# Performance work log

Measured on AMD Instinct MI355X. Metric: run time of the kernel, lower is better.

## Reference

```python
import jax, jax.numpy as jnp
import numpy as np

ATTR_W = 1.0   # attraction_weight
REP_W = 1.0    # repulsion_weight
K_INST = 64    # max number of slice (instance) ids per event


def setup_inputs() -> dict:
    key = jax.random.key(0)
    k1, k2, k3, k4 = jax.random.split(key, 4)
    B, N, D = 4, 4096, 8
    beta = jax.random.normal(k1, (B, N, 1), dtype=jnp.float32)
    embed = jax.random.normal(k2, (B, N, D), dtype=jnp.float32)
    slice_id = jax.random.randint(k3, (B, N), 0, K_INST)
    is_cp = jax.random.randint(k4, (B, N), 0, 2)
    return {"beta": beta, "embed": embed, "slice_id": slice_id, "is_cp": is_cp}


def _per_batch(beta_b, emb_b, sid, cp):
    # beta_b: [N], emb_b: [N, D], sid: [N] int, cp: [N] int
    N = beta_b.shape[0]
    cp_mask = cp == 1
    y = cp_mask.astype(beta_b.dtype)
    pos = jnp.sum(y)
    neg = N - pos
    valid = (pos >= 1) & (neg >= 1)
    # beta BCE-with-logits with detached pos_weight = neg/pos
    pos_weight = jax.lax.stop_gradient(neg / (pos + 1e-6))
    bce = jnp.mean(pos_weight * y * jax.nn.softplus(-beta_b)
                   + (1.0 - y) * jax.nn.softplus(beta_b))
    # attraction: per instance, mean squared distance to first CP hit of that instance
    idx = jnp.arange(N)
    first_cp = jax.ops.segment_min(jnp.where(cp_mask, idx, N), sid, num_segments=K_INST)
    has_cp = first_cp < N                                   # [K]
    cp_emb = emb_b[jnp.clip(first_cp, 0, N - 1)]            # [K, D]
    d2 = jnp.sum((emb_b - cp_emb[sid]) ** 2, axis=-1)       # [N]
    seg_sum = jax.ops.segment_sum(d2, sid, num_segments=K_INST)
    counts = jax.ops.segment_sum(jnp.ones((N,), beta_b.dtype), sid, num_segments=K_INST)
    inst_mean = jnp.where((counts > 0) & has_cp, seg_sum / jnp.maximum(counts, 1.0), 0.0)
    attr = jnp.sum(inst_mean) * ATTR_W
    # repulsion: mean of exp(-d2) over all CP x CP pairs (diagonal included)
    sq = jnp.sum(emb_b * emb_b, axis=-1)                    # [N]
    d2p = jnp.maximum(sq[:, None] + sq[None, :] - 2.0 * (emb_b @ emb_b.T), 0.0)  # [N, N]
    rep_sum = jnp.sum(jnp.exp(-d2p) * (y[:, None] * y[None, :]))
    rep = jnp.where(pos > 1, rep_sum / jnp.maximum(pos * pos, 1.0), 0.0) * REP_W
    total = bce + attr + rep
    return jnp.where(valid, total, 0.0), valid.astype(beta_b.dtype)


def reference(beta, embed, slice_id, is_cp):
    beta2 = beta.squeeze(-1)                                # [B, N]
    totals, valids = jax.vmap(_per_batch)(beta2, embed, slice_id, is_cp)
    count = jnp.sum(valids)
    return jnp.where(count > 0, jnp.sum(totals) / jnp.maximum(count, 1.0), 0.0)
```

## Files before the change

kernel.cpp:

```cpp
#include <hip/hip_runtime.h>
#include <math.h>

#define BB 4
#define NN 4096
#define KK 64
#define IT 1024
#define JT 32
#define K2_BLOCKS (BB * (NN/IT) * (NN/JT))

__global__ __launch_bounds__(1024) void k1(
    const float* __restrict__ beta, const float* __restrict__ embed,
    const int* __restrict__ sid_g, const int* __restrict__ cp_g,
    float* __restrict__ cpemb, float* __restrict__ cpsq,
    float* __restrict__ gbase, float* __restrict__ gpos,
    float* __restrict__ grep, int* __restrict__ gcpn)
{
    const int b    = blockIdx.x;
    const int t    = threadIdx.x;
    const int lane = t & 63;
    const int wid  = t >> 6;

    __shared__ int   s_first[KK];
    __shared__ int   s_counts[KK];
    __shared__ float s_seg[KK];
    __shared__ float s_fe[KK][8];
    __shared__ float r1[16], r2[16], r3[16];
    __shared__ int   s_cpn;

    if (t < KK) { s_first[t] = NN; s_counts[t] = 0; s_seg[t] = 0.f; }
    if (t == 0) s_cpn = 0;
    __syncthreads();

    const int4*   sid4 = (const int4*)(sid_g + (size_t)b * NN);
    const int4*   cp4  = (const int4*)(cp_g + (size_t)b * NN);
    const float4* bt4p = (const float4*)(beta + (size_t)b * NN);
    const float*  emb_b = embed + (size_t)b * NN * 8;

    int4   s4  = sid4[t];
    int4   c4  = cp4[t];
    float4 bt4 = bt4p[t];
    int ssd[4] = {s4.x, s4.y, s4.z, s4.w};
    int cps[4] = {c4.x, c4.y, c4.z, c4.w};
    float bts[4] = {bt4.x, bt4.y, bt4.z, bt4.w};

    float a1 = 0.f, a2 = 0.f;
    int posl = 0;
    int slots[4];

    #pragma unroll
    for (int e = 0; e < 4; ++e) {
        bool is1 = (cps[e] == 1);
        float bt = bts[e];
        float l = __logf(1.f + __expf(-fabsf(bt)));
        if (is1) {
            a1 += l + fmaxf(-bt, 0.f);
            posl++;
            atomicMin(&s_first[ssd[e]], 4 * t + e);
        } else {
            a2 += l + fmaxf(bt, 0.f);
        }
        atomicAdd(&s_counts[ssd[e]], 1);
        unsigned long long m = __ballot(is1);
        int wbase = 0;
        if (lane == 0 && m != 0ull) wbase = atomicAdd(&s_cpn, __popcll(m));
        wbase = __shfl(wbase, 0);
        slots[e] = is1 ? (wbase + __popcll(m & ((1ull << lane) - 1ull))) : -1;
    }

    float pf = (float)posl;
    #pragma unroll
    for (int o = 32; o > 0; o >>= 1) {
        a1 += __shfl_down(a1, o);
        a2 += __shfl_down(a2, o);
        pf += __shfl_down(pf, o);
    }
    if (lane == 0) { r1[wid] = a1; r2[wid] = a2; r3[wid] = pf; }
    __syncthreads();

    if (t < KK) {
        int f = s_first[t]; if (f > NN - 1) f = NN - 1;
        const float4* fp = (const float4*)(emb_b + (size_t)f * 8);
        *(float4*)&s_fe[t][0] = fp[0];
        *(float4*)&s_fe[t][4] = fp[1];
    }
    __syncthreads();

    float* cpe_b = cpemb + (size_t)b * NN * 8;
    float* cpq_b = cpsq + (size_t)b * NN;
    const float S = 1.41421356237f;
    #pragma unroll
    for (int e = 0; e < 4; ++e) {
        int i = 4 * t + e;
        const float4* ep = (const float4*)(emb_b + (size_t)i * 8);
        float4 e0 = ep[0], e1 = ep[1];
        float4 f0 = *(float4*)&s_fe[ssd[e]][0];
        float4 f1 = *(float4*)&s_fe[ssd[e]][4];
        float dx, d2 = 0.f;
        dx = e0.x - f0.x; d2 += dx * dx;
        dx = e0.y - f0.y; d2 += dx * dx;
        dx = e0.z - f0.z; d2 += dx * dx;
        dx = e0.w - f0.w; d2 += dx * dx;
        dx = e1.x - f1.x; d2 += dx * dx;
        dx = e1.y - f1.y; d2 += dx * dx;
        dx = e1.z - f1.z; d2 += dx * dx;
        dx = e1.w - f1.w; d2 += dx * dx;
        atomicAdd(&s_seg[ssd[e]], d2);
        if (slots[e] >= 0) {
            float sq = e0.x*e0.x + e0.y*e0.y + e0.z*e0.z + e0.w*e0.w
                     + e1.x*e1.x + e1.y*e1.y + e1.z*e1.z + e1.w*e1.w;
            float4* op = (float4*)(cpe_b + (size_t)slots[e] * 8);
            op[0] = make_float4(e0.x*S, e0.y*S, e0.z*S, e0.w*S);
            op[1] = make_float4(e1.x*S, e1.y*S, e1.z*S, e1.w*S);
            cpq_b[slots[e]] = sq;
        }
    }
    __syncthreads();

    if (t < KK) {
        int c = s_counts[t], f = s_first[t];
        float attr = (c > 0 && f < NN) ? s_seg[t] / (float)c : 0.f;
        #pragma unroll
        for (int o = 32; o > 0; o >>= 1) attr += __shfl_down(attr, o);
        if (t == 0) {
            float A1 = 0.f, A2 = 0.f, P = 0.f;
            #pragma unroll
            for (int w = 0; w < 16; ++w) { A1 += r1[w]; A2 += r2[w]; P += r3[w]; }
            float neg = (float)NN - P;
            float bce = (neg / (P + 1e-6f) * A1 + A2) * (1.f / (float)NN);
            gbase[b] = bce + attr;
            gpos[b]  = P;
            grep[b]  = 0.f;
            gcpn[b]  = s_cpn;
        }
    }
}

__global__ __launch_bounds__(256) void k2(
    const float* __restrict__ cpemb, const float* __restrict__ cpsq,
    const int* __restrict__ gcpn, float* __restrict__ grep)
{
    const int blk = blockIdx.x;
    const int b   = blk >> 9;
    const int rem = blk & 511;
    const int it  = rem >> 7;
    const int jt  = rem & 127;
    const int t   = threadIdx.x;

    const int pos = gcpn[b];
    if (it * IT >= pos || jt * JT >= pos) return;

    __shared__ float s_je[JT * 8];
    __shared__ float s_jq[JT];
    __shared__ float r[4];

    int jn = pos - jt * JT; if (jn > JT) jn = JT;
    const float* cpe_b = cpemb + (size_t)b * NN * 8;
    const float* cpq_b = cpsq + (size_t)b * NN;

    if (t < 64) {
        int row = t >> 1, half = t & 1;
        if (row < jn) {
            *(float4*)&s_je[row * 8 + half * 4] =
                *(const float4*)(cpe_b + (size_t)(jt * JT + row) * 8 + half * 4);
            if (half == 0) s_jq[row] = cpq_b[jt * JT + row];
        }
    }
    __syncthreads();

    float4 e0[4], e1[4];
    float  nq[4];
    #pragma unroll
    for (int u = 0; u < 4; ++u) {
        int i = it * IT + u * 256 + t;
        bool iv = (i < pos);
        const float4* ip = (const float4*)(cpe_b + (size_t)(iv ? i : 0) * 8);
        e0[u] = ip[0]; e1[u] = ip[1];
        nq[u] = iv ? -cpq_b[i] : -1e30f;
    }

    float sum = 0.f;
    #pragma unroll 2
    for (int j = 0; j < jn; ++j) {
        float4 f0 = *(const float4*)&s_je[j * 8];
        float4 f1 = *(const float4*)&s_je[j * 8 + 4];
        float qj = s_jq[j];
        #pragma unroll
        for (int u = 0; u < 4; ++u) {
            float arg = nq[u] - qj;
            arg = fmaf(e0[u].x, f0.x, arg);
            arg = fmaf(e0[u].y, f0.y, arg);
            arg = fmaf(e0[u].z, f0.z, arg);
            arg = fmaf(e0[u].w, f0.w, arg);
            arg = fmaf(e1[u].x, f1.x, arg);
            arg = fmaf(e1[u].y, f1.y, arg);
            arg = fmaf(e1[u].z, f1.z, arg);
            arg = fmaf(e1[u].w, f1.w, arg);
            arg = fminf(arg, 0.f);
            sum += __expf(arg);
        }
    }
    #pragma unroll
    for (int o = 32; o > 0; o >>= 1) sum += __shfl_down(sum, o);
    if ((t & 63) == 0) r[t >> 6] = sum;
    __syncthreads();
    if (t == 0) atomicAdd(&grep[b], r[0] + r[1] + r[2] + r[3]);
}

__global__ __launch_bounds__(64) void k3(
    const float* __restrict__ gbase, const float* __restrict__ gpos,
    const float* __restrict__ grep, float* __restrict__ out)
{
    if (threadIdx.x == 0) {
        float tot = 0.f, cnt = 0.f;
        #pragma unroll
        for (int b = 0; b < BB; ++b) {
            float P = gpos[b];
            float neg = (float)NN - P;
            bool valid = (P >= 1.f) && (neg >= 1.f);
            float rp = (P > 1.f) ? grep[b] / fmaxf(P * P, 1.f) : 0.f;
            float ttl = gbase[b] + rp;
            if (valid) { tot += ttl; cnt += 1.f; }
        }
        out[0] = (cnt > 0.f) ? tot / cnt : 0.f;
    }
}

extern "C" void kernel_launch(void* const* d_in, const int* in_sizes, int n_in,
                              void* d_out, int out_size, void* d_ws, size_t ws_size,
                              hipStream_t stream) {
    const float* beta     = (const float*)d_in[0];
    const float* embed    = (const float*)d_in[1];
    const int*   slice_id = (const int*)d_in[2];
    const int*   is_cp    = (const int*)d_in[3];
    float* out = (float*)d_out;

    float* cpemb = (float*)d_ws;
    float* cpsq  = cpemb + (size_t)BB * NN * 8;
    float* gbase = cpsq + (size_t)BB * NN;
    float* gpos  = gbase + BB;
    float* grep  = gpos + BB;
    int*   gcpn  = (int*)(grep + BB);

    k1<<<BB, 1024, 0, stream>>>(beta, embed, slice_id, is_cp,
                                cpemb, cpsq, gbase, gpos, grep, gcpn);
    k2<<<K2_BLOCKS, 256, 0, stream>>>(cpemb, cpsq, gcpn, grep);
    k3<<<1, 64, 0, stream>>>(gbase, gpos, grep, out);
}
```

Measured before the change: 87.74 us.

## Move attraction pass into pairwise kernel and fold final reduction into atomics

Removes the third finalize kernel by having each block of the pairwise repulsion kernel atomically add its pre-scaled contribution (validity, 1/P^2, 1/count) directly into the output, which the first kernel zeroes. The attraction distance computation is taken out of the four-block first kernel and run as extra blocks of the second kernel, using per-instance first-CP indices and inverse counts written to global memory. This shortens the serial single-block-per-batch phase and drops a launch, at the cost of re-reading embeddings and slice ids in the new blocks and more float atomics on a single output value, which makes summation order nondeterministic.

```diff
diff --git a/kernel.cpp b/kernel.cpp
--- a/kernel.cpp
+++ b/kernel.cpp
@@ -6,14 +6,18 @@
 #define KK 64
 #define IT 1024
 #define JT 32
-#define K2_BLOCKS (BB * (NN/IT) * (NN/JT))
+#define RB (BB * (NN/IT) * (NN/JT))
+#define ABLK 16
+#define K2_BLOCKS (RB + BB * ABLK)
 
 __global__ __launch_bounds__(1024) void k1(
     const float* __restrict__ beta, const float* __restrict__ embed,
     const int* __restrict__ sid_g, const int* __restrict__ cp_g,
     float* __restrict__ cpemb, float* __restrict__ cpsq,
-    float* __restrict__ gbase, float* __restrict__ gpos,
-    float* __restrict__ grep, int* __restrict__ gcpn)
+    int* __restrict__ gfirst, float* __restrict__ gwinv,
+    float* __restrict__ gval, float* __restrict__ gbce_v,
+    float* __restrict__ grwt, int* __restrict__ gcpn,
+    float* __restrict__ out)
 {
     const int b    = blockIdx.x;
     const int t    = threadIdx.x;
@@ -22,12 +26,10 @@
 
     __shared__ int   s_first[KK];
     __shared__ int   s_counts[KK];
-    __shared__ float s_seg[KK];
-    __shared__ float s_fe[KK][8];
     __shared__ float r1[16], r2[16], r3[16];
     __shared__ int   s_cpn;
 
-    if (t < KK) { s_first[t] = NN; s_counts[t] = 0; s_seg[t] = 0.f; }
+    if (t < KK) { s_first[t] = NN; s_counts[t] = 0; }
     if (t == 0) s_cpn = 0;
     __syncthreads();
 
@@ -35,6 +37,8 @@
     const int4*   cp4  = (const int4*)(cp_g + (size_t)b * NN);
     const float4* bt4p = (const float4*)(beta + (size_t)b * NN);
     const float*  emb_b = embed + (size_t)b * NN * 8;
+    float* cpe_b = cpemb + (size_t)b * NN * 8;
+    float* cpq_b = cpsq + (size_t)b * NN;
 
     int4   s4  = sid4[t];
     int4   c4  = cp4[t];
@@ -45,7 +49,7 @@
 
     float a1 = 0.f, a2 = 0.f;
     int posl = 0;
-    int slots[4];
+    const float S = 1.41421356237f;
 
     #pragma unroll
     for (int e = 0; e < 4; ++e) {
@@ -64,7 +68,17 @@
         int wbase = 0;
         if (lane == 0 && m != 0ull) wbase = atomicAdd(&s_cpn, __popcll(m));
         wbase = __shfl(wbase, 0);
-        slots[e] = is1 ? (wbase + __popcll(m & ((1ull << lane) - 1ull))) : -1;
+        if (is1) {
+            int slot = wbase + __popcll(m & ((1ull << lane) - 1ull));
+            const float4* ep = (const float4*)(emb_b + (size_t)(4 * t + e) * 8);
+            float4 e0 = ep[0], e1 = ep[1];
+            float sq = e0.x*e0.x + e0.y*e0.y + e0.z*e0.z + e0.w*e0.w
+                     + e1.x*e1.x + e1.y*e1.y + e1.z*e1.z + e1.w*e1.w;
+            float4* op = (float4*)(cpe_b + (size_t)slot * 8);
+            op[0] = make_float4(e0.x*S, e0.y*S, e0.z*S, e0.w*S);
+            op[1] = make_float4(e1.x*S, e1.y*S, e1.z*S, e1.w*S);
+            cpq_b[slot] = sq;
+        }
     }
 
     float pf = (float)posl;
@@ -78,23 +92,128 @@
     __syncthreads();
 
     if (t < KK) {
-        int f = s_first[t]; if (f > NN - 1) f = NN - 1;
-        const float4* fp = (const float4*)(emb_b + (size_t)f * 8);
-        *(float4*)&s_fe[t][0] = fp[0];
-        *(float4*)&s_fe[t][4] = fp[1];
-    }
-    __syncthreads();
-
-    float* cpe_b = cpemb + (size_t)b * NN * 8;
-    float* cpq_b = cpsq + (size_t)b * NN;
-    const float S = 1.41421356237f;
-    #pragma unroll
-    for (int e = 0; e < 4; ++e) {
-        int i = 4 * t + e;
+        int f = s_first[t], c = s_counts[t];
+        gfirst[b * KK + t] = f;
+        gwinv[b * KK + t]  = (f < NN && c > 0) ? 1.f / (float)c : 0.f;
+    }
+    if (t == 0) {
+        float A1 = 0.f, A2 = 0.f, P = 0.f;
+        #pragma unroll
+        for (int w = 0; w < 16; ++w) { A1 += r1[w]; A2 += r2[w]; P += r3[w]; }
+        float neg = (float)NN - P;
+        float bce = (neg / (P + 1e-6f) * A1 + A2) * (1.f / (float)NN);
+        float val = ((P >= 1.f) && (neg >= 1.f)) ? 1.f : 0.f;
+        gval[b]   = val;
+        gbce_v[b] = val * bce;
+        grwt[b]   = (P > 1.f) ? val / (P * P) : 0.f;
+        gcpn[b]   = s_cpn;
+        if (b == 0) out[0] = 0.f;
+    }
+}
+
+__global__ __launch_bounds__(256) void k2(
+    const float* __restrict__ embed, const int* __restrict__ sid_g,
+    const float* __restrict__ cpemb, const float* __restrict__ cpsq,
+    const int* __restrict__ gfirst, const float* __restrict__ gwinv,
+    const float* __restrict__ gval, const float* __restrict__ gbce_v,
+    const float* __restrict__ grwt, const int* __restrict__ gcpn,
+    float* __restrict__ out)
+{
+    const int blk = blockIdx.x;
+    const int t   = threadIdx.x;
+
+    __shared__ float s_je[JT * 8];
+    __shared__ float s_jq[JT];
+    __shared__ float s_fe[KK][8];
+    __shared__ float s_winv[KK];
+    __shared__ float s_r[4];
+
+    if (blk < RB) {
+        const int b   = blk >> 9;
+        const int rem = blk & 511;
+        const int it  = rem >> 7;
+        const int jt  = rem & 127;
+        const int pos = gcpn[b];
+        if (it * IT >= pos || jt * JT >= pos) return;
+
+        int jn = pos - jt * JT; if (jn > JT) jn = JT;
+        const float* cpe_b = cpemb + (size_t)b * NN * 8;
+        const float* cpq_b = cpsq + (size_t)b * NN;
+
+        if (t < 64) {
+            int row = t >> 1, half = t & 1;
+            if (row < jn) {
+                *(float4*)&s_je[row * 8 + half * 4] =
+                    *(const float4*)(cpe_b + (size_t)(jt * JT + row) * 8 + half * 4);
+                if (half == 0) s_jq[row] = cpq_b[jt * JT + row];
+            }
+        }
+        __syncthreads();
+
+        float4 e0[4], e1[4];
+        float  nq[4];
+        #pragma unroll
+        for (int u = 0; u < 4; ++u) {
+            int i = it * IT + u * 256 + t;
+            bool iv = (i < pos);
+            const float4* ip = (const float4*)(cpe_b + (size_t)(iv ? i : 0) * 8);
+            e0[u] = ip[0]; e1[u] = ip[1];
+            nq[u] = iv ? -cpq_b[i] : -1e30f;
+        }
+
+        float sum = 0.f;
+        #pragma unroll 2
+        for (int j = 0; j < jn; ++j) {
+            float4 f0 = *(const float4*)&s_je[j * 8];
+            float4 f1 = *(const float4*)&s_je[j * 8 + 4];
+            float qj = s_jq[j];
+            #pragma unroll
+            for (int u = 0; u < 4; ++u) {
+                float arg = nq[u] - qj;
+                arg = fmaf(e0[u].x, f0.x, arg);
+                arg = fmaf(e0[u].y, f0.y, arg);
+                arg = fmaf(e0[u].z, f0.z, arg);
+                arg = fmaf(e0[u].w, f0.w, arg);
+                arg = fmaf(e1[u].x, f1.x, arg);
+                arg = fmaf(e1[u].y, f1.y, arg);
+                arg = fmaf(e1[u].z, f1.z, arg);
+                arg = fmaf(e1[u].w, f1.w, arg);
+                arg = fminf(arg, 0.f);
+                sum += __expf(arg);
+            }
+        }
+        #pragma unroll
+        for (int o = 32; o > 0; o >>= 1) sum += __shfl_down(sum, o);
+        if ((t & 63) == 0) s_r[t >> 6] = sum;
+        __syncthreads();
+        if (t == 0) {
+            float part = s_r[0] + s_r[1] + s_r[2] + s_r[3];
+            float cnt = gval[0] + gval[1] + gval[2] + gval[3];
+            float ic = (cnt > 0.f) ? 1.f / cnt : 0.f;
+            atomicAdd(out, part * grwt[b] * ic);
+        }
+    } else {
+        const int ab  = blk - RB;
+        const int b   = ab >> 4;
+        const int s16 = ab & 15;
+        const float* emb_b = embed + (size_t)b * NN * 8;
+
+        if (t < KK) {
+            int f = gfirst[b * KK + t];
+            if (f > NN - 1) f = NN - 1;
+            const float4* fp = (const float4*)(emb_b + (size_t)f * 8);
+            *(float4*)&s_fe[t][0] = fp[0];
+            *(float4*)&s_fe[t][4] = fp[1];
+            s_winv[t] = gwinv[b * KK + t];
+        }
+        __syncthreads();
+
+        int i = s16 * 256 + t;
+        int sid = sid_g[(size_t)b * NN + i];
         const float4* ep = (const float4*)(emb_b + (size_t)i * 8);
         float4 e0 = ep[0], e1 = ep[1];
-        float4 f0 = *(float4*)&s_fe[ssd[e]][0];
-        float4 f1 = *(float4*)&s_fe[ssd[e]][4];
+        float4 f0 = *(float4*)&s_fe[sid][0];
+        float4 f1 = *(float4*)&s_fe[sid][4];
         float dx, d2 = 0.f;
         dx = e0.x - f0.x; d2 += dx * dx;
         dx = e0.y - f0.y; d2 += dx * dx;
@@ -104,124 +223,20 @@
         dx = e1.y - f1.y; d2 += dx * dx;
         dx = e1.z - f1.z; d2 += dx * dx;
         dx = e1.w - f1.w; d2 += dx * dx;
-        atomicAdd(&s_seg[ssd[e]], d2);
-        if (slots[e] >= 0) {
-            float sq = e0.x*e0.x + e0.y*e0.y + e0.z*e0.z + e0.w*e0.w
-                     + e1.x*e1.x + e1.y*e1.y + e1.z*e1.z + e1.w*e1.w;
-            float4* op = (float4*)(cpe_b + (size_t)slots[e] * 8);
-            op[0] = make_float4(e0.x*S, e0.y*S, e0.z*S, e0.w*S);
-            op[1] = make_float4(e1.x*S, e1.y*S, e1.z*S, e1.w*S);
-            cpq_b[slots[e]] = sq;
-        }
-    }
-    __syncthreads();
-
-    if (t < KK) {
-        int c = s_counts[t], f = s_first[t];
-        float attr = (c > 0 && f < NN) ? s_seg[t] / (float)c : 0.f;
-        #pragma unroll
-        for (int o = 32; o > 0; o >>= 1) attr += __shfl_down(attr, o);
+        float acc = d2 * s_winv[sid];
+
+        #pragma unroll
+        for (int o = 32; o > 0; o >>= 1) acc += __shfl_down(acc, o);
+        if ((t & 63) == 0) s_r[t >> 6] = acc;
+        __syncthreads();
         if (t == 0) {
-            float A1 = 0.f, A2 = 0.f, P = 0.f;
-            #pragma unroll
-            for (int w = 0; w < 16; ++w) { A1 += r1[w]; A2 += r2[w]; P += r3[w]; }
-            float neg = (float)NN - P;
-            float bce = (neg / (P + 1e-6f) * A1 + A2) * (1.f / (float)NN);
-            gbase[b] = bce + attr;
-            gpos[b]  = P;
-            grep[b]  = 0.f;
-            gcpn[b]  = s_cpn;
-        }
-    }
-}
-
-__global__ __launch_bounds__(256) void k2(
-    const float* __restrict__ cpemb, const float* __restrict__ cpsq,
-    const int* __restrict__ gcpn, float* __restrict__ grep)
-{
-    const int blk = blockIdx.x;
-    const int b   = blk >> 9;
-    const int rem = blk & 511;
-    const int it  = rem >> 7;
-    const int jt  = rem & 127;
-    const int t   = threadIdx.x;
-
-    const int pos = gcpn[b];
-    if (it * IT >= pos || jt * JT >= pos) return;
-
-    __shared__ float s_je[JT * 8];
-    __shared__ float s_jq[JT];
-    __shared__ float r[4];
-
-    int jn = pos - jt * JT; if (jn > JT) jn = JT;
-    const float* cpe_b = cpemb + (size_t)b * NN * 8;
-    const float* cpq_b = cpsq + (size_t)b * NN;
-
-    if (t < 64) {
-        int row = t >> 1, half = t & 1;
-        if (row < jn) {
-            *(float4*)&s_je[row * 8 + half * 4] =
-                *(const float4*)(cpe_b + (size_t)(jt * JT + row) * 8 + half * 4);
-            if (half == 0) s_jq[row] = cpq_b[jt * JT + row];
-        }
-    }
-    __syncthreads();
-
-    float4 e0[4], e1[4];
-    float  nq[4];
-    #pragma unroll
-    for (int u = 0; u < 4; ++u) {
-        int i = it * IT + u * 256 + t;
-        bool iv = (i < pos);
-        const float4* ip = (const float4*)(cpe_b + (size_t)(iv ? i : 0) * 8);
-        e0[u] = ip[0]; e1[u] = ip[1];
-        nq[u] = iv ? -cpq_b[i] : -1e30f;
-    }
-
-    float sum = 0.f;
-    #pragma unroll 2
-    for (int j = 0; j < jn; ++j) {
-        float4 f0 = *(const float4*)&s_je[j * 8];
-        float4 f1 = *(const float4*)&s_je[j * 8 + 4];
-        float qj = s_jq[j];
-        #pragma unroll
-        for (int u = 0; u < 4; ++u) {
-            float arg = nq[u] - qj;
-            arg = fmaf(e0[u].x, f0.x, arg);
-            arg = fmaf(e0[u].y, f0.y, arg);
-            arg = fmaf(e0[u].z, f0.z, arg);
-            arg = fmaf(e0[u].w, f0.w, arg);
-            arg = fmaf(e1[u].x, f1.x, arg);
-            arg = fmaf(e1[u].y, f1.y, arg);
-            arg = fmaf(e1[u].z, f1.z, arg);
-            arg = fmaf(e1[u].w, f1.w, arg);
-            arg = fminf(arg, 0.f);
-            sum += __expf(arg);
-        }
-    }
-    #pragma unroll
-    for (int o = 32; o > 0; o >>= 1) sum += __shfl_down(sum, o);
-    if ((t & 63) == 0) r[t >> 6] = sum;
-    __syncthreads();
-    if (t == 0) atomicAdd(&grep[b], r[0] + r[1] + r[2] + r[3]);
-}
-
-__global__ __launch_bounds__(64) void k3(
-    const float* __restrict__ gbase, const float* __restrict__ gpos,
-    const float* __restrict__ grep, float* __restrict__ out)
-{
-    if (threadIdx.x == 0) {
-        float tot = 0.f, cnt = 0.f;
-        #pragma unroll
-        for (int b = 0; b < BB; ++b) {
-            float P = gpos[b];
-            float neg = (float)NN - P;
-            bool valid = (P >= 1.f) && (neg >= 1.f);
-            float rp = (P > 1.f) ? grep[b] / fmaxf(P * P, 1.f) : 0.f;
-            float ttl = gbase[b] + rp;
-            if (valid) { tot += ttl; cnt += 1.f; }
-        }
-        out[0] = (cnt > 0.f) ? tot / cnt : 0.f;
+            float part = s_r[0] + s_r[1] + s_r[2] + s_r[3];
+            float cnt = gval[0] + gval[1] + gval[2] + gval[3];
+            float ic = (cnt > 0.f) ? 1.f / cnt : 0.f;
+            float contrib = part * gval[b];
+            if (s16 == 0) contrib += gbce_v[b];
+            atomicAdd(out, contrib * ic);
+        }
     }
 }
 
@@ -234,15 +249,19 @@
     const int*   is_cp    = (const int*)d_in[3];
     float* out = (float*)d_out;
 
-    float* cpemb = (float*)d_ws;
-    float* cpsq  = cpemb + (size_t)BB * NN * 8;
-    float* gbase = cpsq + (size_t)BB * NN;
-    float* gpos  = gbase + BB;
-    float* grep  = gpos + BB;
-    int*   gcpn  = (int*)(grep + BB);
+    float* cpemb  = (float*)d_ws;
+    float* cpsq   = cpemb + (size_t)BB * NN * 8;
+    float* gwinv  = cpsq + (size_t)BB * NN;
+    float* gval   = gwinv + BB * KK;
+    float* gbce_v = gval + BB;
+    float* grwt   = gbce_v + BB;
+    int*   gfirst = (int*)(grwt + BB);
+    int*   gcpn   = gfirst + BB * KK;
 
     k1<<<BB, 1024, 0, stream>>>(beta, embed, slice_id, is_cp,
-                                cpemb, cpsq, gbase, gpos, grep, gcpn);
-    k2<<<K2_BLOCKS, 256, 0, stream>>>(cpemb, cpsq, gcpn, grep);
-    k3<<<1, 64, 0, stream>>>(gbase, gpos, grep, out);
+                                cpemb, cpsq, gfirst, gwinv,
+                                gval, gbce_v, grwt, gcpn, out);
+    k2<<<K2_BLOCKS, 256, 0, stream>>>(embed, slice_id, cpemb, cpsq,
+                                      gfirst, gwinv, gval, gbce_v,
+                                      grwt, gcpn, out);
 }
```

Measured after the change: 82.98 us, median of 2. -5.4%, faster.
